# Optimization experiments

Hardware: AMD Instinct MI355X
Metric: run time of the kernel (lower is better)

The kernel has to match this reference:

```python
import jax, jax.numpy as jnp
import numpy as np

NUM_HEADS = 16
ROPE_BASE = 10000.0


def rotate_half(x):
    d = x.shape[-1] // 2
    return jnp.concatenate([-x[..., d:], x[..., :d]], axis=-1)


def setup_inputs() -> dict:
    key = jax.random.key(0)
    ks = jax.random.split(key, 6)
    B, S, H = 2, 2048, 1024
    scale = 1.0 / np.sqrt(H)  # ~xavier for square matrices
    x = jax.random.normal(ks[0], (B, S, H), dtype=jnp.float32)
    Wq = jax.random.normal(ks[1], (H, H), dtype=jnp.float32) * scale
    Wk = jax.random.normal(ks[2], (H, H), dtype=jnp.float32) * scale
    Wv = jax.random.normal(ks[3], (H, H), dtype=jnp.float32) * scale
    Wo = jax.random.normal(ks[4], (H, H), dtype=jnp.float32) * scale
    # learnable bias, tril-initialized as in the torch module
    bias = jnp.tril(jax.random.normal(ks[5], (S, S), dtype=jnp.float32) * 0.02)
    return {"x": x, "Wq": Wq, "Wk": Wk, "Wv": Wv, "Wo": Wo, "bias": bias}


def reference(x, Wq, Wk, Wv, Wo, bias):
    B, S, H = x.shape
    nh = NUM_HEADS
    hd = H // nh

    # projections (torch Linear: y = x @ W.T), split heads -> [B, nh, S, hd]
    q = (x @ Wq.T).reshape(B, S, nh, hd).transpose(0, 2, 1, 3)
    k = (x @ Wk.T).reshape(B, S, nh, hd).transpose(0, 2, 1, 3)
    v = (x @ Wv.T).reshape(B, S, nh, hd).transpose(0, 2, 1, 3)

    # rotary embeddings, position_ids = arange(S)
    inv_freq = 1.0 / (ROPE_BASE ** (jnp.arange(0, hd, 2, dtype=jnp.float32) / hd))
    t = jnp.arange(S, dtype=jnp.float32)
    freqs = t[:, None] * inv_freq[None, :]          # [S, hd/2]
    emb = jnp.concatenate([freqs, freqs], axis=-1)  # [S, hd]
    cos = jnp.cos(emb).astype(x.dtype)
    sin = jnp.sin(emb).astype(x.dtype)
    q = q * cos + rotate_half(q) * sin
    k = k * cos + rotate_half(k) * sin

    # scores + learnable bias + causal mask
    scores = jnp.einsum('bhqd,bhkd->bhqk', q, k) / np.float32(np.sqrt(hd))
    scores = scores + bias[:S, :S][None, None, :, :]
    causal = jnp.tril(jnp.ones((S, S), dtype=bool))
    scores = jnp.where(causal, scores, -jnp.inf)

    attn = jax.nn.softmax(scores, axis=-1)
    out = jnp.einsum('bhqk,bhkd->bhqd', attn, v)
    out = out.transpose(0, 2, 1, 3).reshape(B, S, H)
    return out @ Wo.T, attn
```

## Files before the change

### kernel.cpp

```cpp
#include <hip/hip_runtime.h>
#include <hip/hip_bf16.h>
#include <math.h>


typedef __attribute__((ext_vector_type(8))) short bx8;
typedef __attribute__((ext_vector_type(4))) short sx4;
typedef __attribute__((ext_vector_type(4))) float fx4;
typedef __attribute__((ext_vector_type(4))) float f4v;

#define MFMA_BF16(a, b, c) __builtin_amdgcn_mfma_f32_16x16x32_bf16(a, b, c, 0, 0, 0)
#define LOG2E 1.44269504088896340736f

__device__ __forceinline__ short f2bf(float f) {
    union { float f; unsigned u; } v; v.f = f;
    unsigned u = v.u;
    u += 0x7fffu + ((u >> 16) & 1u);
    return (short)(u >> 16);
}
__device__ __forceinline__ float u2f(unsigned u) {
    union { unsigned u; float f; } v; v.u = u; return v.f;
}

__device__ __forceinline__ bx8 pack8(f4v a, f4v b) {
    bx8 r;
    r[0] = f2bf(a[0]); r[1] = f2bf(a[1]); r[2] = f2bf(a[2]); r[3] = f2bf(a[3]);
    r[4] = f2bf(b[0]); r[5] = f2bf(b[1]); r[6] = f2bf(b[2]); r[7] = f2bf(b[3]);
    return r;
}

__device__ __forceinline__ void gload_lds16(const short* g, short* l) {
    __builtin_amdgcn_global_load_lds(
        (const __attribute__((address_space(1))) void*)g,
        (__attribute__((address_space(3))) void*)l, 16, 0, 0);
}

__global__ __launch_bounds__(256) void cast_kernel(
        const float* __restrict__ x, const float* __restrict__ Wq,
        const float* __restrict__ Wk, const float* __restrict__ Wv,
        const float* __restrict__ Wo, const float* __restrict__ bias,
        short* __restrict__ dst, float* __restrict__ biasF)
{
    const size_t M1 = 1u << 20;
    if (blockIdx.x < 4096) {
        const size_t e0 = ((size_t)blockIdx.x * 256 + threadIdx.x) * 8;
        const float* src; size_t off;
        if (e0 < 4 * M1) { src = x; off = e0; }
        else {
            const int j = (int)((e0 - 4 * M1) >> 20);
            src = (j == 0) ? Wq : (j == 1) ? Wk : (j == 2) ? Wv : Wo;
            off = (e0 - 4 * M1) & (M1 - 1);
        }
        f4v a = *(const f4v*)(src + off);
        f4v b = *(const f4v*)(src + off + 4);
        *(bx8*)(dst + e0) = pack8(a, b);
    } else {
        const size_t e0 = ((size_t)(blockIdx.x - 4096) * 256 + threadIdx.x) * 8;
        f4v a = *(const f4v*)(bias + e0);
        f4v b = *(const f4v*)(bias + e0 + 4);
        #pragma unroll
        for (int i = 0; i < 4; ++i) { a[i] *= LOG2E; b[i] *= LOG2E; }
        *(f4v*)(biasF + e0) = a;
        *(f4v*)(biasF + e0 + 4) = b;
    }
}

__global__ void rope_table_kernel(float* __restrict__ cosT, float* __restrict__ sinT) {
    int i = blockIdx.x * 256 + threadIdx.x;
    if (i >= 2048 * 64) return;
    int s = i >> 6, d = i & 63;
    int fi = d & 31;
    float inv_freq = powf(10000.0f, -(float)fi / 32.0f);
    float ang = (float)s * inv_freq;
    cosT[i] = cosf(ang);
    sinT[i] = sinf(ang);
}

template<int OUTPROJ>
__global__ __launch_bounds__(256) void gemm128(
        const short* __restrict__ A, const short* __restrict__ W0,
        const short* __restrict__ W1, const short* __restrict__ W2,
        const float* __restrict__ cosT, const float* __restrict__ sinT,
        void* __restrict__ Out)
{
    __shared__ short As[128][64];
    __shared__ short Bs[128][64];
    const int bm = blockIdx.x, bn = blockIdx.y, z = blockIdx.z;
    const short* W = OUTPROJ ? W0 : (z == 0 ? W0 : (z == 1 ? W1 : W2));
    const int tid = threadIdx.x, w = tid >> 6, lane = tid & 63;
    const int cl = lane & 15, lg = lane >> 4;
    const int srow = lane >> 3;
    const int schunk = (lane & 7) ^ srow;

    fx4 acc[4][4];
    #pragma unroll
    for (int mi = 0; mi < 4; ++mi)
        #pragma unroll
        for (int ni = 0; ni < 4; ++ni) acc[mi][ni] = (fx4){0.f, 0.f, 0.f, 0.f};

    const int wr = (w >> 1) * 64, wc = (w & 1) * 64;

    for (int k0 = 0; k0 < 1024; k0 += 64) {
        __syncthreads();
        #pragma unroll
        for (int i = 0; i < 4; ++i) {
            const int rbase = w * 32 + i * 8;
            gload_lds16(A + (size_t)(bm * 128 + rbase + srow) * 1024 + k0 + schunk * 8,
                        &As[rbase][0]);
            gload_lds16(W + (size_t)(bn * 128 + rbase + srow) * 1024 + k0 + schunk * 8,
                        &Bs[rbase][0]);
        }
        __syncthreads();
        #pragma unroll
        for (int kk = 0; kk < 2; ++kk) {
            bx8 af[4], bf[4];
            #pragma unroll
            for (int i = 0; i < 4; ++i) {
                const int ra = wr + i * 16 + cl;
                af[i] = *(const bx8*)&As[ra][((kk * 4 + lg) ^ (ra & 7)) * 8];
                const int rb = wc + i * 16 + cl;
                bf[i] = *(const bx8*)&Bs[rb][((kk * 4 + lg) ^ (rb & 7)) * 8];
            }
            #pragma unroll
            for (int mi = 0; mi < 4; ++mi)
                #pragma unroll
                for (int ni = 0; ni < 4; ++ni)
                    acc[mi][ni] = MFMA_BF16(af[mi], bf[ni], acc[mi][ni]);
        }
    }

    #pragma unroll
    for (int mi = 0; mi < 4; ++mi) {
        #pragma unroll
        for (int reg = 0; reg < 4; ++reg) {
            const int r = bm * 128 + wr + mi * 16 + (lg << 2) + reg;
            if constexpr (OUTPROJ) {
                #pragma unroll
                for (int ni = 0; ni < 4; ++ni) {
                    const int col = bn * 128 + wc + ni * 16 + cl;
                    ((float*)Out)[(size_t)r * 1024 + col] = acc[mi][ni][reg];
                }
            } else {
                const int b = r >> 11, s = r & 2047;
                const int h = bn * 2 + (wc >> 6);
                short* dst = (short*)Out + (size_t)z * 32 * 2048 * 64
                           + (size_t)((b * 16 + h) * 2048 + s) * 64;
                #pragma unroll
                for (int ni = 0; ni < 4; ++ni) {
                    const int d = ni * 16 + cl;
                    float v = acc[mi][ni][reg];
                    if (z <= 1) {
                        const float cs = cosT[s * 64 + d], sn = sinT[s * 64 + d];
                        const float partner = acc[mi][ni ^ 2][reg];
                        const float rot = (d < 32) ? -partner : partner;
                        v = v * cs + rot * sn;
                        if (z == 0) v *= 0.125f * LOG2E;
                    }
                    dst[d] = f2bf(v);
                }
            }
        }
    }
}

__global__ __launch_bounds__(256, 3) void attn_kernel(
        const short* __restrict__ Q, const short* __restrict__ K,
        const short* __restrict__ V, const float* __restrict__ biasF,
        float* __restrict__ attn_out, short* __restrict__ o_buf)
{
    const int S = 2048;
    const int bid = blockIdx.x;
    const int xcd = bid & 7, rr_ = bid >> 3;
    const int bh = xcd * 4 + (rr_ & 3);
    const int qt = 31 - (rr_ >> 2);
    const int h = bh & 15, b = bh >> 4;
    const int tid = threadIdx.x, w = tid >> 6, lane = tid & 63;
    const int cl = lane & 15, lg = lane >> 4;
    const size_t base = (size_t)bh * S * 64;
    const int NT = qt + 1;

    __shared__ short Ks[2][64][64];
    __shared__ short Vt[2][64][72];
    __shared__ short P[4][16][136];

    const int krow8 = lane >> 3, kchk = (lane & 7) ^ krow8;
    const int vrow = tid >> 2, vd0 = (tid & 3) * 16;

    const short* qp = Q + base + (size_t)(qt * 64 + w * 16 + cl) * 64 + lg * 8;
    const bx8 qf0 = *(const bx8*)qp;
    const bx8 qf1 = *(const bx8*)(qp + 32);
    const int qr  = qt * 64 + w * 16 + cl;
    const int sq0 = qt * 64 + w * 16 + (lg << 2);
    const float* brow = biasF + (size_t)qr * 2048;
    const size_t strip_base = ((size_t)bh * S + qt * 64 + w * 16) * S;

#define STAGEK(BUF, t)                                                            \
    { gload_lds16(K + base + (size_t)((t) * 64 + w * 16 + krow8) * 64 + kchk * 8, \
                  &Ks[BUF][w * 16][0]);                                           \
      gload_lds16(K + base + (size_t)((t) * 64 + w * 16 + 8 + krow8) * 64 + kchk * 8, \
                  &Ks[BUF][w * 16 + 8][0]); }

#define LOADB(BR, t)                                                              \
    { _Pragma("unroll") for (int n = 0; n < 4; ++n)                               \
        BR[n] = *(const f4v*)(brow + (t) * 64 + n * 16 + (lg << 2)); }

#define QKT(BUF, BR, SACC)                                                        \
    { const int cs_ = cl & 7;                                                     \
      _Pragma("unroll") for (int n = 0; n < 4; ++n) {                             \
        bx8 a0 = *(const bx8*)&Ks[BUF][n * 16 + cl][(lg ^ cs_) * 8];              \
        bx8 a1 = *(const bx8*)&Ks[BUF][n * 16 + cl][((4 + lg) ^ cs_) * 8];        \
        SACC[n] = MFMA_BF16(a0, qf0, BR[n]);                                      \
        SACC[n] = MFMA_BF16(a1, qf1, SACC[n]); } }

#define COMP_A(BUF, BR, t)                                                        \
    { fx4 sacc[4]; QKT(BUF, BR, sacc);                                            \
      _Pragma("unroll") for (int n = 0; n < 4; ++n)                               \
        _Pragma("unroll") for (int e = 0; e < 4; ++e) {                           \
          const int kc = (t) * 64 + n * 16 + (lg << 2) + e;                       \
          lsum[n] += (kc <= qr) ? exp2f(sacc[n][e]) : 0.f; } }

#define LOADVr(V0, V1, t)                                                         \
    { const short* vp = V + base + (size_t)((t) * 64 + vrow) * 64 + vd0;          \
      V0 = *(const bx8*)vp; V1 = *(const bx8*)(vp + 8); }

#define VSTORE(V0, V1, BUF)                                                       \
    { _Pragma("unroll") for (int j = 0; j < 8; ++j) Vt[BUF][vd0 + j][vrow] = V0[j]; \
      _Pragma("unroll") for (int j = 0; j < 8; ++j) Vt[BUF][vd0 + 8 + j][vrow] = V1[j]; }

#define COMP_B(KBUF, BR, VBUF, t)                                                 \
    { fx4 sacc[4]; QKT(KBUF, BR, sacc);                                           \
      _Pragma("unroll") for (int n = 0; n < 4; ++n) {                             \
        sx4 pb;                                                                   \
        _Pragma("unroll") for (int e = 0; e < 4; ++e) {                           \
          const int kc = (t) * 64 + n * 16 + (lg << 2) + e;                       \
          const float p = (kc <= qr) ? exp2f(sacc[n][e] - L2) : 0.f;              \
          pb[e] = f2bf(p); }                                                      \
        *(sx4*)&P[w][cl][((t) & 1) * 64 + n * 16 + (lg << 2)] = pb; }             \
      _Pragma("unroll") for (int kk = 0; kk < 2; ++kk) {                          \
        bx8 pa = *(const bx8*)&P[w][cl][((t) & 1) * 64 + kk * 32 + lg * 8];       \
        _Pragma("unroll") for (int n = 0; n < 4; ++n) {                           \
          bx8 vb = *(const bx8*)&Vt[VBUF][n * 16 + cl][kk * 32 + lg * 8];         \
          oacc[n] = MFMA_BF16(pa, vb, oacc[n]); } } }

#define FLUSH2(tp)                                                                \
    { _Pragma("unroll") for (int rp = 0; rp < 16; rp += 2) {                      \
        const int row = rp + (lane >> 5), col = (lane & 31) * 4;                  \
        const unsigned* ps = (const unsigned*)&P[w][row][col];                    \
        const unsigned px = ps[0], py = ps[1];                                    \
        f4v o; o[0] = u2f(px << 16); o[1] = u2f(px & 0xffff0000u);                \
        o[2] = u2f(py << 16); o[3] = u2f(py & 0xffff0000u);                       \
        *(f4v*)(attn_out + strip_base + (size_t)row * S + (tp) * 64 + col) = o; } }

#define FLUSH1(tp)                                                                \
    { _Pragma("unroll") for (int rp = 0; rp < 16; rp += 4) {                      \
        const int row = rp + (lane >> 4), col = (lane & 15) * 4;                  \
        const unsigned* ps = (const unsigned*)&P[w][row][col];                    \
        const unsigned px = ps[0], py = ps[1];                                    \
        f4v o; o[0] = u2f(px << 16); o[1] = u2f(px & 0xffff0000u);                \
        o[2] = u2f(py << 16); o[3] = u2f(py & 0xffff0000u);                       \
        *(f4v*)(attn_out + strip_base + (size_t)row * S + (tp) * 64 + col) = o; } }

    float lsum[4] = {0.f, 0.f, 0.f, 0.f};
    f4v bA[4], bB[4];

    STAGEK(0, 0); LOADB(bA, 0);
    __syncthreads();
    int t = 0;
    for (; t + 1 < NT; t += 2) {
        STAGEK(1, t + 1); LOADB(bB, t + 1);
        COMP_A(0, bA, t);
        __syncthreads();
        if (t + 2 < NT) { STAGEK(0, t + 2); LOADB(bA, t + 2); }
        COMP_A(1, bB, t + 1);
        __syncthreads();
    }
    if (t < NT) COMP_A(0, bA, t);

    float l = (lsum[0] + lsum[1]) + (lsum[2] + lsum[3]);
    l += __shfl_xor(l, 16);
    l += __shfl_xor(l, 32);
    const float L2 = __log2f(l);

    fx4 oacc[4];
    #pragma unroll
    for (int n = 0; n < 4; n++) oacc[n] = (fx4){0.f, 0.f, 0.f, 0.f};

    bx8 vA0, vA1, vB0, vB1;
    __syncthreads();
    STAGEK(0, 0); LOADB(bA, 0); LOADVr(vA0, vA1, 0);
    __syncthreads();
    VSTORE(vA0, vA1, 0);
    __syncthreads();
    t = 0;
    for (; t + 1 < NT; t += 2) {
        STAGEK(1, t + 1); LOADB(bB, t + 1); LOADVr(vB0, vB1, t + 1);
        COMP_B(0, bA, 0, t);
        VSTORE(vB0, vB1, 1);
        __syncthreads();
        if (t + 2 < NT) { STAGEK(0, t + 2); LOADB(bA, t + 2); LOADVr(vA0, vA1, t + 2); }
        COMP_B(1, bB, 1, t + 1);
        FLUSH2(t);
        if (t + 2 < NT) VSTORE(vA0, vA1, 0);
        __syncthreads();
    }
    if (t < NT) { COMP_B(0, bA, 0, t); FLUSH1(t); }

    #pragma unroll
    for (int reg = 0; reg < 4; reg++) {
        const int sq = sq0 + reg;
        #pragma unroll
        for (int n = 0; n < 4; n++) {
            const int d = n * 16 + cl;
            o_buf[(size_t)(b * 2048 + sq) * 1024 + h * 64 + d] = f2bf(oacc[n][reg]);
        }
    }

    const int c0 = (qt + 1) * 64;
    if (c0 < S) {
        const f4v z = (f4v){0.f, 0.f, 0.f, 0.f};
        for (int r = w; r < 64; r += 4) {
            float* dst = attn_out + ((size_t)bh * S + qt * 64 + r) * S;
            for (int cc = c0 + lane * 4; cc < S; cc += 256)
                *(f4v*)(dst + cc) = z;
        }
    }
#undef STAGEK
#undef LOADB
#undef QKT
#undef COMP_A
#undef LOADVr
#undef VSTORE
#undef COMP_B
#undef FLUSH2
#undef FLUSH1
}

extern "C" void kernel_launch(void* const* d_in, const int* in_sizes, int n_in,
                              void* d_out, int out_size, void* d_ws, size_t ws_size,
                              hipStream_t stream) {
    const float* x    = (const float*)d_in[0];
    const float* Wq   = (const float*)d_in[1];
    const float* Wk   = (const float*)d_in[2];
    const float* Wv   = (const float*)d_in[3];
    const float* Wo   = (const float*)d_in[4];
    const float* bias = (const float*)d_in[5];

    float* out  = (float*)d_out;
    float* attn = out + (size_t)2 * 2048 * 1024;

    char* ws = (char*)d_ws;
    const size_t M1 = 1u << 20;
    short* x_bf    = (short*)ws;
    short* wq_bf   = x_bf + 4 * M1;
    short* wk_bf   = wq_bf + M1;
    short* wv_bf   = wk_bf + M1;
    short* wo_bf   = wv_bf + M1;
    float* biasF   = (float*)(ws + 16 * M1);
    float* cosT    = (float*)(ws + 32 * M1);
    float* sinT    = cosT + 2048 * 64;
    short* q_rope  = (short*)(ws + 33 * M1);
    short* k_rope  = q_rope + 4 * M1;
    short* v_bf    = k_rope + 4 * M1;
    short* o_buf   = x_bf;

    cast_kernel<<<6144, 256, 0, stream>>>(x, Wq, Wk, Wv, Wo, bias, x_bf, biasF);
    rope_table_kernel<<<512, 256, 0, stream>>>(cosT, sinT);
    gemm128<0><<<dim3(32, 8, 3), 256, 0, stream>>>(x_bf, wq_bf, wk_bf, wv_bf,
                                                   cosT, sinT, q_rope);
    attn_kernel<<<1024, 256, 0, stream>>>(q_rope, k_rope, v_bf, biasF, attn, o_buf);
    gemm128<1><<<dim3(32, 8, 1), 256, 0, stream>>>(o_buf, wo_bf, wo_bf, wo_bf,
                                                   cosT, sinT, out);
}
```

Before: 282.3 us.

## Load K directly to registers in pass one and use nontemporal attn stores

The first pass, which computes the softmax row sums, now loads K fragments and bias straight from global memory into registers with double buffering. This replaces the LDS staging and drops the block-wide barriers from that pass. All stores of the attention matrix, including the zero fill of the masked upper region, become nontemporal stores so the large output stream does not pollute the cache. In exchange, register pressure rises and each wave issues redundant global K loads instead of sharing them through LDS.

```diff
diff --git a/kernel.cpp b/kernel.cpp
--- a/kernel.cpp
+++ b/kernel.cpp
@@ -193,6 +193,23 @@
     const float* brow = biasF + (size_t)qr * 2048;
     const size_t strip_base = ((size_t)bh * S + qt * 64 + w * 16) * S;
 
+#define LOADKB(KARR, BARR, t)                                                    \
+    { _Pragma("unroll") for (int n = 0; n < 4; ++n) {                            \
+        const short* kp = K + base + (size_t)((t) * 64 + n * 16 + cl) * 64 + lg * 8; \
+        KARR[n][0] = *(const bx8*)kp; KARR[n][1] = *(const bx8*)(kp + 32); }     \
+      _Pragma("unroll") for (int n = 0; n < 4; ++n)                              \
+        BARR[n] = *(const f4v*)(brow + (t) * 64 + n * 16 + (lg << 2)); }
+
+#define COMP_A(KARR, BARR, t)                                                    \
+    { fx4 sacc[4];                                                               \
+      _Pragma("unroll") for (int n = 0; n < 4; ++n) {                            \
+        sacc[n] = MFMA_BF16(KARR[n][0], qf0, (fx4)BARR[n]);                      \
+        sacc[n] = MFMA_BF16(KARR[n][1], qf1, sacc[n]); }                         \
+      _Pragma("unroll") for (int n = 0; n < 4; ++n)                              \
+        _Pragma("unroll") for (int e = 0; e < 4; ++e) {                          \
+          const int kc = (t) * 64 + n * 16 + (lg << 2) + e;                      \
+          lsum[n] += (kc <= qr) ? exp2f(sacc[n][e]) : 0.f; } }
+
 #define STAGEK(BUF, t)                                                            \
     { gload_lds16(K + base + (size_t)((t) * 64 + w * 16 + krow8) * 64 + kchk * 8, \
                   &Ks[BUF][w * 16][0]);                                           \
@@ -210,13 +227,6 @@
         bx8 a1 = *(const bx8*)&Ks[BUF][n * 16 + cl][((4 + lg) ^ cs_) * 8];        \
         SACC[n] = MFMA_BF16(a0, qf0, BR[n]);                                      \
         SACC[n] = MFMA_BF16(a1, qf1, SACC[n]); } }
-
-#define COMP_A(BUF, BR, t)                                                        \
-    { fx4 sacc[4]; QKT(BUF, BR, sacc);                                            \
-      _Pragma("unroll") for (int n = 0; n < 4; ++n)                               \
-        _Pragma("unroll") for (int e = 0; e < 4; ++e) {                           \
-          const int kc = (t) * 64 + n * 16 + (lg << 2) + e;                       \
-          lsum[n] += (kc <= qr) ? exp2f(sacc[n][e]) : 0.f; } }
 
 #define LOADVr(V0, V1, t)                                                         \
     { const short* vp = V + base + (size_t)((t) * 64 + vrow) * 64 + vd0;          \
@@ -248,7 +258,8 @@
         const unsigned px = ps[0], py = ps[1];                                    \
         f4v o; o[0] = u2f(px << 16); o[1] = u2f(px & 0xffff0000u);                \
         o[2] = u2f(py << 16); o[3] = u2f(py & 0xffff0000u);                       \
-        *(f4v*)(attn_out + strip_base + (size_t)row * S + (tp) * 64 + col) = o; } }
+        __builtin_nontemporal_store(o,                                            \
+            (f4v*)(attn_out + strip_base + (size_t)row * S + (tp) * 64 + col)); } }
 
 #define FLUSH1(tp)                                                                \
     { _Pragma("unroll") for (int rp = 0; rp < 16; rp += 4) {                      \
@@ -257,23 +268,24 @@
         const unsigned px = ps[0], py = ps[1];                                    \
         f4v o; o[0] = u2f(px << 16); o[1] = u2f(px & 0xffff0000u);                \
         o[2] = u2f(py << 16); o[3] = u2f(py & 0xffff0000u);                       \
-        *(f4v*)(attn_out + strip_base + (size_t)row * S + (tp) * 64 + col) = o; } }
+        __builtin_nontemporal_store(o,                                            \
+            (f4v*)(attn_out + strip_base + (size_t)row * S + (tp) * 64 + col)); } }
 
     float lsum[4] = {0.f, 0.f, 0.f, 0.f};
-    f4v bA[4], bB[4];
-
-    STAGEK(0, 0); LOADB(bA, 0);
-    __syncthreads();
-    int t = 0;
-    for (; t + 1 < NT; t += 2) {
-        STAGEK(1, t + 1); LOADB(bB, t + 1);
-        COMP_A(0, bA, t);
-        __syncthreads();
-        if (t + 2 < NT) { STAGEK(0, t + 2); LOADB(bA, t + 2); }
-        COMP_A(1, bB, t + 1);
-        __syncthreads();
-    }
-    if (t < NT) COMP_A(0, bA, t);
+
+    {
+        bx8 kA[4][2], kB[4][2];
+        f4v bA[4], bB[4];
+        LOADKB(kA, bA, 0);
+        int t = 0;
+        for (; t + 1 < NT; t += 2) {
+            LOADKB(kB, bB, t + 1);
+            COMP_A(kA, bA, t);
+            if (t + 2 < NT) LOADKB(kA, bA, t + 2);
+            COMP_A(kB, bB, t + 1);
+        }
+        if (t < NT) COMP_A(kA, bA, t);
+    }
 
     float l = (lsum[0] + lsum[1]) + (lsum[2] + lsum[3]);
     l += __shfl_xor(l, 16);
@@ -284,13 +296,13 @@
     #pragma unroll
     for (int n = 0; n < 4; n++) oacc[n] = (fx4){0.f, 0.f, 0.f, 0.f};
 
+    f4v bA[4], bB[4];
     bx8 vA0, vA1, vB0, vB1;
-    __syncthreads();
     STAGEK(0, 0); LOADB(bA, 0); LOADVr(vA0, vA1, 0);
     __syncthreads();
     VSTORE(vA0, vA1, 0);
     __syncthreads();
-    t = 0;
+    int t = 0;
     for (; t + 1 < NT; t += 2) {
         STAGEK(1, t + 1); LOADB(bB, t + 1); LOADVr(vB0, vB1, t + 1);
         COMP_B(0, bA, 0, t);
@@ -320,13 +332,14 @@
         for (int r = w; r < 64; r += 4) {
             float* dst = attn_out + ((size_t)bh * S + qt * 64 + r) * S;
             for (int cc = c0 + lane * 4; cc < S; cc += 256)
-                *(f4v*)(dst + cc) = z;
-        }
-    }
+                __builtin_nontemporal_store(z, (f4v*)(dst + cc));
+        }
+    }
+#undef LOADKB
+#undef COMP_A
 #undef STAGEK
 #undef LOADB
 #undef QKT
-#undef COMP_A
 #undef LOADVr
 #undef VSTORE
 #undef COMP_B
```

New measurement: 284.7 us. No clear change (+0.8%).
